# Optimization experiments

Measured on AMD Instinct MI355X. Metric: run time of the kernel, lower is better.

## Reference

```python
import jax, jax.numpy as jnp
import numpy as np

H, D = 8, 16            # num_heads, head_size
IN = H * D              # hgt_in_dim = 128
NT, ET = 3, 4           # node types, edge types (hard-coded in module)
N_DRUG, N_DIS, N_PROT = 10000, 10000, 30000
N = N_DRUG + N_DIS + N_PROT
E = 400000
LAYERS = 2
SQRT_D = float(np.sqrt(D))

# homogeneous node-type vector (presorted by type, as dgl.to_homogeneous yields)
NTYPE = jnp.concatenate([
    jnp.zeros(N_DRUG, jnp.int32),
    jnp.ones(N_DIS, jnp.int32),
    jnp.full((N_PROT,), 2, jnp.int32),
])


def typed_linear(x, types, W):
    # x: (M, in), W: (T, in, out), types: (M,) -> y[m] = x[m] @ W[types[m]]
    out = jnp.zeros((x.shape[0], W.shape[2]), x.dtype)
    for t in range(W.shape[0]):
        out = out + jnp.where((types == t)[:, None], x @ W[t], 0.0)
    return out


def hgt_conv(x, src, dst, etype, Wk, Wq, Wv, Wa, rel_att, rel_msg, pri, skip):
    # type-specific K/Q/V projections
    k = typed_linear(x, NTYPE, Wk).reshape(N, H, D)
    q = typed_linear(x, NTYPE, Wq).reshape(N, H, D)
    v = typed_linear(x, NTYPE, Wv).reshape(N, H, D)
    ke, qe, ve = k[src], q[dst], v[src]          # (E, H, D) gathers

    # per-edge-type relation transforms (vectorized over heads)
    kw = jnp.zeros_like(ke)
    mw = jnp.zeros_like(ve)
    for t in range(ET):
        sel = (etype == t)[:, None, None]
        kw = kw + jnp.where(sel, jnp.einsum('ehd,hdo->eho', ke, rel_att[:, t]), 0.0)
        mw = mw + jnp.where(sel, jnp.einsum('ehd,hdo->eho', ve, rel_msg[:, t]), 0.0)

    # attention logits: (kw . q) * relation_pri[head, etype] / sqrt(D)
    a = (kw * qe).sum(-1) * pri.T[etype] / SQRT_D  # (E, H)

    # edge softmax grouped by destination node, per head
    amax = jax.ops.segment_max(a, dst, num_segments=N)      # (N, H)
    ea = jnp.exp(a - amax[dst])
    esum = jax.ops.segment_sum(ea, dst, num_segments=N)
    attn = ea / esum[dst]                                   # (E, H)

    # weighted message aggregation (scatter-add over dst)
    m = mw * attn[..., None]                                 # (E, H, D)
    h = jax.ops.segment_sum(m, dst, num_segments=N).reshape(N, IN)

    # output projection (dropout = identity in eval) + sigmoid-skip residual
    h = typed_linear(h, NTYPE, Wa)
    alpha = jax.nn.sigmoid(skip)[NTYPE][:, None]
    return h * alpha + x * (1.0 - alpha)


def setup_inputs() -> dict:
    key = jax.random.key(0)
    ks = jax.random.split(key, 12)
    s = 0.05
    return {
        "drug_feature": jax.random.normal(ks[0], (N_DRUG, IN), jnp.float32),
        "disease_feature": jax.random.normal(ks[1], (N_DIS, IN), jnp.float32),
        "protein_feature": jax.random.normal(ks[2], (N_PROT, IN), jnp.float32),
        "src": jax.random.randint(ks[3], (E,), 0, N, dtype=jnp.int32),
        "dst": jax.random.randint(ks[4], (E,), 0, N, dtype=jnp.int32),
        "etype": jnp.sort(jax.random.randint(ks[5], (E,), 0, ET, dtype=jnp.int32)),
        "Wk": jax.random.normal(ks[6], (NT, IN, IN), jnp.float32) * s,
        "Wq": jax.random.normal(ks[7], (NT, IN, IN), jnp.float32) * s,
        "Wv": jax.random.normal(ks[8], (NT, IN, IN), jnp.float32) * s,
        "Wa": jax.random.normal(ks[9], (NT, IN, IN), jnp.float32) * s,
        "rel_att": jax.random.normal(ks[10], (H, ET, D, D), jnp.float32) * 0.1,
        "rel_msg": jax.random.normal(ks[11], (H, ET, D, D), jnp.float32) * 0.1,
        "pri": jnp.ones((H, ET), jnp.float32),
        "skip": jnp.ones((NT,), jnp.float32),
    }


def reference(drug_feature, disease_feature, protein_feature, src, dst, etype,
              Wk, Wq, Wv, Wa, rel_att, rel_msg, pri, skip):
    x = jnp.concatenate([drug_feature, disease_feature, protein_feature], axis=0)
    # ModuleList holds the SAME conv instance -> shared weights across layers
    for _ in range(LAYERS):
        x = hgt_conv(x, src, dst, etype, Wk, Wq, Wv, Wa, rel_att, rel_msg, pri, skip)
    return x
```

## Files before the change

### kernel.cpp

```cpp
#include <hip/hip_runtime.h>

#define N_NODE 50000
#define N_EDGE 400000
#define INF    128

#define FUSED_BLOCKS 1536

#define TILES0 313
#define TILES1 313
#define TILES2 938
#define PTILES 1564
#define PBLOCKS2 782

#define SB_CONCAT 2048
#define SB_COUNT  1563
#define SB_TWT    768
#define SB_TRMSG  32
#define SB_TOTAL  (SB_CONCAT + SB_COUNT + SB_TWT + SB_TRMSG)

typedef __bf16 bf16x8 __attribute__((ext_vector_type(8)));
typedef float  f32x4  __attribute__((ext_vector_type(4)));

__device__ __forceinline__ void seg_decode(int b, int& ty, int& base, int& nrows) {
  if (b < TILES0)            { ty = 0; base = b * 32;                      nrows = 10000 - base; }
  else if (b < TILES0+TILES1){ ty = 1; base = 10000 + (b - TILES0) * 32;   nrows = 20000 - base; }
  else                       { ty = 2; base = 20000 + (b - TILES0-TILES1)*32; nrows = 50000 - base; }
  if (nrows > 32) nrows = 32;
}

__device__ __forceinline__ float blo(unsigned u) { return __uint_as_float(u << 16); }
__device__ __forceinline__ float bhi(unsigned u) { return __uint_as_float(u & 0xffff0000u); }
__device__ __forceinline__ unsigned bpack(float lo, float hi) {
  unsigned a = __float_as_uint(lo), b = __float_as_uint(hi);
  a = (a + 0x7fffu + ((a >> 16) & 1u)) >> 16;
  b = (b + 0x7fffu + ((b >> 16) & 1u)) & 0xffff0000u;
  return a | b;
}
__device__ __forceinline__ unsigned short b16(float v) {
  unsigned u = __float_as_uint(v);
  return (unsigned short)((u + 0x7fffu + ((u >> 16) & 1u)) >> 16);
}
__device__ __forceinline__ bf16x8 ld_frag(const unsigned short* p) {
  uint4 u = *reinterpret_cast<const uint4*>(p);
  return __builtin_bit_cast(bf16x8, u);
}

__global__ __launch_bounds__(256) void k_setup(const float* __restrict__ dr,
                                               const float* __restrict__ di,
                                               const float* __restrict__ pr,
                                               float* __restrict__ x,
                                               unsigned short* __restrict__ xh,
                                               const int* __restrict__ dst,
                                               int* __restrict__ deg,
                                               const float* __restrict__ Wk,
                                               const float* __restrict__ Wq,
                                               const float* __restrict__ Wv,
                                               const float* __restrict__ Wa,
                                               unsigned short* __restrict__ WT,
                                               const float* __restrict__ rm,
                                               float* __restrict__ AmT) {
  int b = blockIdx.x;
  if (b < SB_CONCAT) {
    for (int i = b * 256 + threadIdx.x; i < N_NODE * 32; i += SB_CONCAT * 256) {
      int row = i >> 5;
      float4 val;
      if (row < 10000)      val = ((const float4*)dr)[i];
      else if (row < 20000) val = ((const float4*)di)[i - 10000*32];
      else                  val = ((const float4*)pr)[i - 20000*32];
      ((float4*)x)[i] = val;
      ((uint2*)xh)[i] = make_uint2(bpack(val.x, val.y), bpack(val.z, val.w));
    }
  } else if (b < SB_CONCAT + SB_COUNT) {
    int e = (b - SB_CONCAT) * 256 + threadIdx.x;
    if (e < N_EDGE) atomicAdd(&deg[dst[e]], 1);
  } else if (b < SB_CONCAT + SB_COUNT + SB_TWT) {
    int idx = (b - SB_CONCAT - SB_COUNT) * 256 + threadIdx.x;
    if (idx < 196608) {
      int mt = idx >> 14;
      int within = idx & 16383;
      int o = within >> 7, ii = within & 127;
      int mat = mt / 3, ty = mt % 3;
      const float* W = (mat == 0) ? Wk : (mat == 1) ? Wq : (mat == 2) ? Wv : Wa;
      WT[idx] = b16(W[ty * 16384 + ii * 128 + o]);
    }
  } else {
    int i = (b - SB_CONCAT - SB_COUNT - SB_TWT) * 256 + threadIdx.x;
    int di2 = i & 15, doo = (i >> 4) & 15, ty = (i >> 8) & 3, hh = i >> 10;
    AmT[i] = rm[((hh * 4 + ty) * 16 + di2) * 16 + doo];
  }
}

__global__ __launch_bounds__(1024) void k_scan(const int* __restrict__ deg,
                                               int* __restrict__ off, int* __restrict__ cur) {
  __shared__ int part[1024];
  int t = threadIdx.x;
  int c0 = t * 49;
  int c1 = c0 + 49; if (c1 > N_NODE) c1 = N_NODE;
  int s = 0;
  for (int i = c0; i < c1; ++i) s += deg[i];
  part[t] = s;
  __syncthreads();
  for (int ofs = 1; ofs < 1024; ofs <<= 1) {
    int v = (t >= ofs) ? part[t - ofs] : 0;
    __syncthreads();
    part[t] += v;
    __syncthreads();
  }
  int run = (t == 0) ? 0 : part[t - 1];
  for (int i = c0; i < c1; ++i) { off[i] = run; cur[i] = run; run += deg[i]; }
  if (t == 1023) off[N_NODE] = part[1023];
}

__global__ __launch_bounds__(256) void k_fill(const int* __restrict__ dst,
                                              const int* __restrict__ src,
                                              const int* __restrict__ etp,
                                              int* __restrict__ cur, int* __restrict__ est) {
  int e = blockIdx.x * 256 + threadIdx.x;
  if (e < N_EDGE) {
    int p = atomicAdd(&cur[dst[e]], 1);
    est[p] = (src[e] << 2) | etp[e];
  } else if (e < N_EDGE + 64) {
    est[e] = 0;
  }
}

__global__ __launch_bounds__(256) void k_qkv(const unsigned short* __restrict__ xh,
                                             const unsigned short* __restrict__ WT,
                                             const float* __restrict__ rel_att,
                                             const float* __restrict__ pri,
                                             uint2* __restrict__ kvb,
                                             uint4* __restrict__ qab) {
  __shared__ unsigned short qsh[2][32][136];
  int w = threadIdx.x >> 6, l = threadIdx.x & 63;
  int r16 = l & 15, ks = l >> 4;
  int t = w >> 1, ch = w & 1;
  int tile = blockIdx.x * 2 + t;
  int ty, base, wrows;
  seg_decode(tile, ty, base, wrows);
  int row0 = base;

  bf16x8 a[2][4];
#pragma unroll
  for (int st = 0; st < 2; ++st) {
    const unsigned short* xrow = xh + (size_t)(row0 + st * 16 + r16) * 128 + ks * 8;
#pragma unroll
    for (int kk = 0; kk < 4; ++kk) a[st][kk] = ld_frag(xrow + kk * 32);
  }

  const unsigned short* WK = WT + (size_t)(0 * 3 + ty) * 16384;
  const unsigned short* WQ = WT + (size_t)(1 * 3 + ty) * 16384;
  const unsigned short* WV = WT + (size_t)(2 * 3 + ty) * 16384;

#pragma unroll 1
  for (int ct = ch * 4; ct < ch * 4 + 4; ++ct) {
    int o = ct * 16 + r16;
    bf16x8 fbk[4], fbq[4], fbv[4];
#pragma unroll
    for (int kk = 0; kk < 4; ++kk) {
      fbk[kk] = ld_frag(WK + (size_t)o * 128 + ks * 8 + kk * 32);
      fbq[kk] = ld_frag(WQ + (size_t)o * 128 + ks * 8 + kk * 32);
      fbv[kk] = ld_frag(WV + (size_t)o * 128 + ks * 8 + kk * 32);
    }
#pragma unroll
    for (int st = 0; st < 2; ++st) {
      f32x4 ak = {0.f,0.f,0.f,0.f}, aq = {0.f,0.f,0.f,0.f}, av = {0.f,0.f,0.f,0.f};
#pragma unroll
      for (int kk = 0; kk < 4; ++kk) {
        ak = __builtin_amdgcn_mfma_f32_16x16x32_bf16(a[st][kk], fbk[kk], ak, 0, 0, 0);
        aq = __builtin_amdgcn_mfma_f32_16x16x32_bf16(a[st][kk], fbq[kk], aq, 0, 0, 0);
        av = __builtin_amdgcn_mfma_f32_16x16x32_bf16(a[st][kk], fbv[kk], av, 0, 0, 0);
      }
#pragma unroll
      for (int r = 0; r < 4; ++r) {
        int rrel = st * 16 + ks * 4 + r;
        float kn = __shfl_xor(ak[r], 1);
        float vn = __shfl_xor(av[r], 1);
        qsh[t][rrel][o] = b16(aq[r]);
        if (rrel < wrows && (l & 1) == 0) {
          size_t p = (size_t)(row0 + rrel);
          kvb[p * 64 + (o >> 1)] = make_uint2(bpack(ak[r], kn), bpack(av[r], vn));
        }
      }
    }
  }
  __syncthreads();

  int h = l >> 3, j = l & 7;
  float4 prh = ((const float4*)pri)[h];
  float prs[4] = { prh.x * 0.25f, prh.y * 0.25f, prh.z * 0.25f, prh.w * 0.25f };
  int nd0 = ch * 16;
  int lim = wrows - nd0; if (lim > 16) lim = 16;
  for (int i = 0; i < lim; ++i) {
    int nd = nd0 + i;
    unsigned u[8];
    *(uint4*)&u[0] = *(uint4*)&qsh[t][nd][h * 16 + 0];
    *(uint4*)&u[4] = *(uint4*)&qsh[t][nd][h * 16 + 8];
    float qf[16];
#pragma unroll
    for (int q2 = 0; q2 < 8; ++q2) { qf[2*q2] = blo(u[q2]); qf[2*q2+1] = bhi(u[q2]); }
    unsigned pk[4];
#pragma unroll
    for (int t4 = 0; t4 < 4; ++t4) {
      const float* Ar = rel_att + (((h * 4 + t4) * 16) + 2 * j) * 16;
      float ax = 0.f, ay = 0.f;
#pragma unroll
      for (int o = 0; o < 16; ++o) {
        ax += Ar[o] * qf[o];
        ay += Ar[16 + o] * qf[o];
      }
      pk[t4] = bpack(ax * prs[t4], ay * prs[t4]);
    }
    qab[(size_t)(row0 + nd) * 64 + l] = make_uint4(pk[0], pk[1], pk[2], pk[3]);
  }
}

__global__ __launch_bounds__(256)
__attribute__((amdgpu_waves_per_eu(3, 6)))
void k_fused(const uint2* __restrict__ kvb,
             const uint4* __restrict__ qab,
             const int* __restrict__ off,
             const int* __restrict__ est,
             const float* __restrict__ AmT,
             unsigned* __restrict__ hbh) {
  __shared__ float accs[4][4][128];
  int w = threadIdx.x >> 6, l = threadIdx.x & 63;
  int h = l >> 3, j = l & 7;

  for (int n = blockIdx.x * 4 + w; n < N_NODE; n += FUSED_BLOCKS * 4) {
    int o0 = off[n], o1 = off[n + 1];

    uint4 qu = qab[(size_t)n * 64 + l];
    float2 qa0 = make_float2(blo(qu.x), bhi(qu.x));
    float2 qa1 = make_float2(blo(qu.y), bhi(qu.y));
    float2 qa2 = make_float2(blo(qu.z), bhi(qu.z));
    float2 qa3 = make_float2(blo(qu.w), bhi(qu.w));

    float ssum = 0.f;
    float2 z = make_float2(0.f, 0.f);
    float2 at0 = z, at1 = z, at2 = z, at3 = z;

#define PROC(KV, TY, VALID) { \
    int ty = (TY) & 3; \
    float kx = blo((KV).x), ky = bhi((KV).x); \
    float2 qat = (ty==0)?qa0:(ty==1)?qa1:(ty==2)?qa2:qa3; \
    float part = kx*qat.x + ky*qat.y; \
    part += __shfl_xor(part, 1); \
    part += __shfl_xor(part, 2); \
    part += __shfl_xor(part, 4); \
    float wgt = (VALID) ? __expf(part) : 0.f; \
    ssum += wgt; \
    float vx = blo((KV).y), vy = bhi((KV).y); \
    float w0=(ty==0)?wgt:0.f, w1=(ty==1)?wgt:0.f, w2=(ty==2)?wgt:0.f, w3=(ty==3)?wgt:0.f; \
    at0.x += w0*vx; at0.y += w0*vy; \
    at1.x += w1*vx; at1.y += w1*vy; \
    at2.x += w2*vx; at2.y += w2*vy; \
    at3.x += w3*vx; at3.y += w3*vy; }

    for (int b0 = o0; b0 < o1; b0 += 64) {
      int cnt = o1 - b0; if (cnt > 64) cnt = 64;
      int stv = est[b0 + (l < cnt ? l : cnt - 1)];
      int t0 = __shfl(stv, 0);
      int t1 = __shfl(stv, 1 < cnt ? 1 : 0);
      uint2 kv0 = kvb[(size_t)(t0 >> 2) * 64 + l];
      uint2 kv1 = kvb[(size_t)(t1 >> 2) * 64 + l];
      for (int i = 0; i < cnt; i += 2) {
        bool more = (i + 2) < cnt;
        int n0 = 0, n1 = 0; uint2 kn0, kn1;
        if (more) {
          n0 = __shfl(stv, i + 2);
          n1 = __shfl(stv, (i + 3) < cnt ? (i + 3) : (i + 2));
          kn0 = kvb[(size_t)(n0 >> 2) * 64 + l];
          kn1 = kvb[(size_t)(n1 >> 2) * 64 + l];
        }
        PROC(kv0, t0, true)
        PROC(kv1, t1, (i + 1) < cnt)
        if (more) { t0 = n0; t1 = n1; kv0 = kn0; kv1 = kn1; }
      }
    }
#undef PROC

    float inv = (ssum > 0.f) ? 1.f / ssum : 0.f;
    at0.x *= inv; at0.y *= inv;
    at1.x *= inv; at1.y *= inv;
    at2.x *= inv; at2.y *= inv;
    at3.x *= inv; at3.y *= inv;

    ((float2*)&accs[w][0][0])[l] = at0;
    ((float2*)&accs[w][1][0])[l] = at1;
    ((float2*)&accs[w][2][0])[l] = at2;
    ((float2*)&accs[w][3][0])[l] = at3;

    float ox = 0.f, oy = 0.f;
#pragma unroll
    for (int ty = 0; ty < 4; ++ty) {
      const float4* AmR = (const float4*)(AmT + ((h * 4 + ty) * 16) * 16);
#pragma unroll
      for (int d4 = 0; d4 < 4; ++d4) {
        float4 ac = *((float4*)&accs[w][ty][h * 16 + d4 * 4]);
        float4 m0 = AmR[(2 * j) * 4 + d4];
        float4 m1 = AmR[(2 * j + 1) * 4 + d4];
        ox += m0.x * ac.x + m0.y * ac.y + m0.z * ac.z + m0.w * ac.w;
        oy += m1.x * ac.x + m1.y * ac.y + m1.z * ac.z + m1.w * ac.w;
      }
    }
    hbh[(size_t)n * 64 + l] = bpack(ox, oy);
  }
}

__global__ __launch_bounds__(256) void k_outqkv(const unsigned short* __restrict__ hbh,
                                                const unsigned short* __restrict__ WT,
                                                const float* __restrict__ skipv,
                                                const float* __restrict__ rel_att,
                                                const float* __restrict__ pri,
                                                float* __restrict__ xio,
                                                uint2* __restrict__ kvb,
                                                uint4* __restrict__ qab) {
  __shared__ unsigned short qsh[2][32][136];
  int w = threadIdx.x >> 6, l = threadIdx.x & 63;
  int r16 = l & 15, ks = l >> 4;
  int t = w >> 1, ch = w & 1;
  int tile = blockIdx.x * 2 + t;
  int ty, base, wrows;
  seg_decode(tile, ty, base, wrows);
  int row0 = base;

  {
    bf16x8 a[2][4];
#pragma unroll
    for (int st = 0; st < 2; ++st) {
      const unsigned short* hrow = hbh + (size_t)(row0 + st * 16 + r16) * 128 + ks * 8;
#pragma unroll
      for (int kk = 0; kk < 4; ++kk) a[st][kk] = ld_frag(hrow + kk * 32);
    }
    const unsigned short* WA = WT + (size_t)(3 * 3 + ty) * 16384;
    float alpha = 1.f / (1.f + __expf(-skipv[ty]));
    float beta = 1.f - alpha;
#pragma unroll 1
    for (int ct = ch * 4; ct < ch * 4 + 4; ++ct) {
      int o = ct * 16 + r16;
      bf16x8 ba[4];
#pragma unroll
      for (int kk = 0; kk < 4; ++kk)
        ba[kk] = ld_frag(WA + (size_t)o * 128 + ks * 8 + kk * 32);
#pragma unroll
      for (int st = 0; st < 2; ++st) {
        f32x4 acc = {0.f,0.f,0.f,0.f};
#pragma unroll
        for (int kk = 0; kk < 4; ++kk)
          acc = __builtin_amdgcn_mfma_f32_16x16x32_bf16(a[st][kk], ba[kk], acc, 0, 0, 0);
#pragma unroll
        for (int r = 0; r < 4; ++r) {
          int rrel = st * 16 + ks * 4 + r;
          size_t p = (size_t)(row0 + rrel) * 128 + o;
          float nx = 0.f;
          if (rrel < wrows) {
            nx = acc[r] * alpha + xio[p] * beta;
            xio[p] = nx;
          }
          qsh[t][rrel][o] = b16(nx);
        }
      }
    }
  }
  __syncthreads();

  bf16x8 a[2][4];
#pragma unroll
  for (int st = 0; st < 2; ++st)
#pragma unroll
    for (int kk = 0; kk < 4; ++kk)
      a[st][kk] = ld_frag(&qsh[t][st * 16 + r16][ks * 8 + kk * 32]);
  __syncthreads();

  const unsigned short* WK = WT + (size_t)(0 * 3 + ty) * 16384;
  const unsigned short* WQ = WT + (size_t)(1 * 3 + ty) * 16384;
  const unsigned short* WV = WT + (size_t)(2 * 3 + ty) * 16384;
#pragma unroll 1
  for (int ct = ch * 4; ct < ch * 4 + 4; ++ct) {
    int o = ct * 16 + r16;
    bf16x8 fbk[4], fbq[4], fbv[4];
#pragma unroll
    for (int kk = 0; kk < 4; ++kk) {
      fbk[kk] = ld_frag(WK + (size_t)o * 128 + ks * 8 + kk * 32);
      fbq[kk] = ld_frag(WQ + (size_t)o * 128 + ks * 8 + kk * 32);
      fbv[kk] = ld_frag(WV + (size_t)o * 128 + ks * 8 + kk * 32);
    }
#pragma unroll
    for (int st = 0; st < 2; ++st) {
      f32x4 ak = {0.f,0.f,0.f,0.f}, aq = {0.f,0.f,0.f,0.f}, av = {0.f,0.f,0.f,0.f};
#pragma unroll
      for (int kk = 0; kk < 4; ++kk) {
        ak = __builtin_amdgcn_mfma_f32_16x16x32_bf16(a[st][kk], fbk[kk], ak, 0, 0, 0);
        aq = __builtin_amdgcn_mfma_f32_16x16x32_bf16(a[st][kk], fbq[kk], aq, 0, 0, 0);
        av = __builtin_amdgcn_mfma_f32_16x16x32_bf16(a[st][kk], fbv[kk], av, 0, 0, 0);
      }
#pragma unroll
      for (int r = 0; r < 4; ++r) {
        int rrel = st * 16 + ks * 4 + r;
        float kn = __shfl_xor(ak[r], 1);
        float vn = __shfl_xor(av[r], 1);
        qsh[t][rrel][o] = b16(aq[r]);
        if (rrel < wrows && (l & 1) == 0) {
          size_t p = (size_t)(row0 + rrel);
          kvb[p * 64 + (o >> 1)] = make_uint2(bpack(ak[r], kn), bpack(av[r], vn));
        }
      }
    }
  }
  __syncthreads();

  int h = l >> 3, j = l & 7;
  float4 prh = ((const float4*)pri)[h];
  float prs[4] = { prh.x * 0.25f, prh.y * 0.25f, prh.z * 0.25f, prh.w * 0.25f };
  int nd0 = ch * 16;
  int lim = wrows - nd0; if (lim > 16) lim = 16;
  for (int i = 0; i < lim; ++i) {
    int nd = nd0 + i;
    unsigned u[8];
    *(uint4*)&u[0] = *(uint4*)&qsh[t][nd][h * 16 + 0];
    *(uint4*)&u[4] = *(uint4*)&qsh[t][nd][h * 16 + 8];
    float qf[16];
#pragma unroll
    for (int q2 = 0; q2 < 8; ++q2) { qf[2*q2] = blo(u[q2]); qf[2*q2+1] = bhi(u[q2]); }
    unsigned pk[4];
#pragma unroll
    for (int t4 = 0; t4 < 4; ++t4) {
      const float* Ar = rel_att + (((h * 4 + t4) * 16) + 2 * j) * 16;
      float ax = 0.f, ay = 0.f;
#pragma unroll
      for (int o = 0; o < 16; ++o) {
        ax += Ar[o] * qf[o];
        ay += Ar[16 + o] * qf[o];
      }
      pk[t4] = bpack(ax * prs[t4], ay * prs[t4]);
    }
    qab[(size_t)(row0 + nd) * 64 + l] = make_uint4(pk[0], pk[1], pk[2], pk[3]);
  }
}

__global__ __launch_bounds__(256) void k_out(const unsigned short* __restrict__ hbh,
                                             const unsigned short* __restrict__ WT,
                                             const float* __restrict__ skipv,
                                             float* __restrict__ xio) {
  int w = threadIdx.x >> 6, l = threadIdx.x & 63;
  int r16 = l & 15, ks = l >> 4;
  int t = w >> 1, ch = w & 1;
  int tile = blockIdx.x * 2 + t;
  int ty, base, wrows;
  seg_decode(tile, ty, base, wrows);
  int row0 = base;

  bf16x8 a[2][4];
#pragma unroll
  for (int st = 0; st < 2; ++st) {
    const unsigned short* hrow = hbh + (size_t)(row0 + st * 16 + r16) * 128 + ks * 8;
#pragma unroll
    for (int kk = 0; kk < 4; ++kk) a[st][kk] = ld_frag(hrow + kk * 32);
  }

  const unsigned short* WA = WT + (size_t)(3 * 3 + ty) * 16384;
  float alpha = 1.f / (1.f + __expf(-skipv[ty]));
  float beta = 1.f - alpha;

#pragma unroll 1
  for (int ct = ch * 4; ct < ch * 4 + 4; ++ct) {
    int o = ct * 16 + r16;
    bf16x8 ba[4];
#pragma unroll
    for (int kk = 0; kk < 4; ++kk)
      ba[kk] = ld_frag(WA + (size_t)o * 128 + ks * 8 + kk * 32);
#pragma unroll
    for (int st = 0; st < 2; ++st) {
      f32x4 acc = {0.f,0.f,0.f,0.f};
#pragma unroll
      for (int kk = 0; kk < 4; ++kk)
        acc = __builtin_amdgcn_mfma_f32_16x16x32_bf16(a[st][kk], ba[kk], acc, 0, 0, 0);
#pragma unroll
      for (int r = 0; r < 4; ++r) {
        int rrel = st * 16 + ks * 4 + r;
        if (rrel < wrows) {
          size_t p = (size_t)(row0 + rrel) * 128 + o;
          xio[p] = acc[r] * alpha + xio[p] * beta;
        }
      }
    }
  }
}

extern "C" void kernel_launch(void* const* d_in, const int* in_sizes, int n_in,
                              void* d_out, int out_size, void* d_ws, size_t ws_size,
                              hipStream_t stream) {
  const float* drug = (const float*)d_in[0];
  const float* dis  = (const float*)d_in[1];
  const float* prot = (const float*)d_in[2];
  const int* src    = (const int*)d_in[3];
  const int* dst    = (const int*)d_in[4];
  const int* etp    = (const int*)d_in[5];
  const float* Wk   = (const float*)d_in[6];
  const float* Wq   = (const float*)d_in[7];
  const float* Wv   = (const float*)d_in[8];
  const float* Wa   = (const float*)d_in[9];
  const float* rel_att = (const float*)d_in[10];
  const float* rel_msg = (const float*)d_in[11];
  const float* pri  = (const float*)d_in[12];
  const float* skip = (const float*)d_in[13];
  float* x = (float*)d_out;

  char* w = (char*)d_ws;
  uint2*          kvb = (uint2*)(w + 0);
  unsigned*       hbh = (unsigned*)(w + 25600000);
  uint4*          qab = (uint4*)(w + 38400000);
  unsigned short* xh  = (unsigned short*)(w + 89600000);
  unsigned short* WT  = (unsigned short*)(w + 102400000);
  float*          AmT = (float*)(w + 102793216);
  int*            off = (int*)(w + 102825984);
  int*            est = (int*)(w + 103026048);
  int*            deg = (int*)(w + 25600000);
  int*            cur = (int*)(w + 25800064);

  (void)hipMemsetAsync(deg, 0, N_NODE * sizeof(int), stream);
  k_setup<<<SB_TOTAL, 256, 0, stream>>>(drug, dis, prot, x, xh, dst, deg,
                                        Wk, Wq, Wv, Wa, WT, rel_msg, AmT);
  k_scan<<<1, 1024, 0, stream>>>(deg, off, cur);
  k_fill<<<(N_EDGE + 64 + 255) / 256, 256, 0, stream>>>(dst, src, etp, cur, est);

  k_qkv<<<PBLOCKS2, 256, 0, stream>>>(xh, WT, rel_att, pri, kvb, qab);
  k_fused<<<FUSED_BLOCKS, 256, 0, stream>>>(kvb, qab, off, est, AmT, hbh);
  k_outqkv<<<PBLOCKS2, 256, 0, stream>>>((const unsigned short*)hbh, WT, skip,
                                         rel_att, pri, x, kvb, qab);
  k_fused<<<FUSED_BLOCKS, 256, 0, stream>>>(kvb, qab, off, est, AmT, hbh);
  k_out<<<PBLOCKS2, 256, 0, stream>>>((const unsigned short*)hbh, WT, skip, x);
}
```

Measured before the change: 689.3 us.

## Process two destination nodes per wavefront with 32-lane halves and 16-byte gathers

The fused attention/aggregation kernel now splits each 64-lane wavefront into two 32-lane halves, each handling its own destination node. Every lane gathers a uint4 (four K and four V elements) per edge, so the dot-product reduction drops one shuffle stage, and the output projection computes four outputs per lane. The goal is to double per-lane work, widen memory transactions and cut per-node shuffle and loop overhead. The cost is divergence when the two nodes in a wave have different degrees, because the loop runs to the larger degree with masked edges. The est padding is also extended to 128 entries to cover the out-of-range reads that masked slots can make.

```diff
diff --git a/kernel.cpp b/kernel.cpp
--- a/kernel.cpp
+++ b/kernel.cpp
@@ -119,7 +119,7 @@
   if (e < N_EDGE) {
     int p = atomicAdd(&cur[dst[e]], 1);
     est[p] = (src[e] << 2) | etp[e];
-  } else if (e < N_EDGE + 64) {
+  } else if (e < N_EDGE + 128) {
     est[e] = 0;
   }
 }
@@ -222,88 +222,103 @@
              const int* __restrict__ est,
              const float* __restrict__ AmT,
              unsigned* __restrict__ hbh) {
-  __shared__ float accs[4][4][128];
+  __shared__ float accs[4][2][4][128];
+  const uint4* kv4 = (const uint4*)kvb;
   int w = threadIdx.x >> 6, l = threadIdx.x & 63;
-  int h = l >> 3, j = l & 7;
-
-  for (int n = blockIdx.x * 4 + w; n < N_NODE; n += FUSED_BLOCKS * 4) {
+  int half = l >> 5, m = l & 31;
+  int h = m >> 2, q4 = (m & 3) * 4;
+  int hbase = l & 32;
+
+  for (int nb = blockIdx.x * 8 + w * 2; nb < N_NODE; nb += FUSED_BLOCKS * 8) {
+    int n = nb + half;
     int o0 = off[n], o1 = off[n + 1];
-
-    uint4 qu = qab[(size_t)n * 64 + l];
-    float2 qa0 = make_float2(blo(qu.x), bhi(qu.x));
-    float2 qa1 = make_float2(blo(qu.y), bhi(qu.y));
-    float2 qa2 = make_float2(blo(qu.z), bhi(qu.z));
-    float2 qa3 = make_float2(blo(qu.w), bhi(qu.w));
+    int deg = o1 - o0;
+    int degmax = max(deg, __shfl_xor(deg, 32));
+
+    uint4 qu0 = qab[(size_t)n * 64 + 2 * m];
+    uint4 qu1 = qab[(size_t)n * 64 + 2 * m + 1];
+    float4 qa0 = make_float4(blo(qu0.x), bhi(qu0.x), blo(qu1.x), bhi(qu1.x));
+    float4 qa1 = make_float4(blo(qu0.y), bhi(qu0.y), blo(qu1.y), bhi(qu1.y));
+    float4 qa2 = make_float4(blo(qu0.z), bhi(qu0.z), blo(qu1.z), bhi(qu1.z));
+    float4 qa3 = make_float4(blo(qu0.w), bhi(qu0.w), blo(qu1.w), bhi(qu1.w));
 
     float ssum = 0.f;
-    float2 z = make_float2(0.f, 0.f);
-    float2 at0 = z, at1 = z, at2 = z, at3 = z;
-
-#define PROC(KV, TY, VALID) { \
-    int ty = (TY) & 3; \
-    float kx = blo((KV).x), ky = bhi((KV).x); \
-    float2 qat = (ty==0)?qa0:(ty==1)?qa1:(ty==2)?qa2:qa3; \
-    float part = kx*qat.x + ky*qat.y; \
+    float4 z = make_float4(0.f, 0.f, 0.f, 0.f);
+    float4 at0 = z, at1 = z, at2 = z, at3 = z;
+
+#define PROC(KV, T, VALID) { \
+    int ty = (T) & 3; \
+    float k0 = blo((KV).x), k1 = bhi((KV).x), k2 = blo((KV).z), k3 = bhi((KV).z); \
+    float4 qat = (ty==0)?qa0:(ty==1)?qa1:(ty==2)?qa2:qa3; \
+    float part = k0*qat.x + k1*qat.y + k2*qat.z + k3*qat.w; \
     part += __shfl_xor(part, 1); \
     part += __shfl_xor(part, 2); \
-    part += __shfl_xor(part, 4); \
     float wgt = (VALID) ? __expf(part) : 0.f; \
     ssum += wgt; \
-    float vx = blo((KV).y), vy = bhi((KV).y); \
+    float v0 = blo((KV).y), v1 = bhi((KV).y), v2 = blo((KV).w), v3 = bhi((KV).w); \
     float w0=(ty==0)?wgt:0.f, w1=(ty==1)?wgt:0.f, w2=(ty==2)?wgt:0.f, w3=(ty==3)?wgt:0.f; \
-    at0.x += w0*vx; at0.y += w0*vy; \
-    at1.x += w1*vx; at1.y += w1*vy; \
-    at2.x += w2*vx; at2.y += w2*vy; \
-    at3.x += w3*vx; at3.y += w3*vy; }
-
-    for (int b0 = o0; b0 < o1; b0 += 64) {
-      int cnt = o1 - b0; if (cnt > 64) cnt = 64;
-      int stv = est[b0 + (l < cnt ? l : cnt - 1)];
-      int t0 = __shfl(stv, 0);
-      int t1 = __shfl(stv, 1 < cnt ? 1 : 0);
-      uint2 kv0 = kvb[(size_t)(t0 >> 2) * 64 + l];
-      uint2 kv1 = kvb[(size_t)(t1 >> 2) * 64 + l];
-      for (int i = 0; i < cnt; i += 2) {
-        bool more = (i + 2) < cnt;
-        int n0 = 0, n1 = 0; uint2 kn0, kn1;
+    at0.x += w0*v0; at0.y += w0*v1; at0.z += w0*v2; at0.w += w0*v3; \
+    at1.x += w1*v0; at1.y += w1*v1; at1.z += w1*v2; at1.w += w1*v3; \
+    at2.x += w2*v0; at2.y += w2*v1; at2.z += w2*v2; at2.w += w2*v3; \
+    at3.x += w3*v0; at3.y += w3*v1; at3.z += w3*v2; at3.w += w3*v3; }
+
+    for (int b0 = 0; b0 < degmax; b0 += 32) {
+      int cnt = deg - b0; if (cnt > 32) cnt = 32; if (cnt < 0) cnt = 0;
+      int cmax = degmax - b0; if (cmax > 32) cmax = 32;
+      int cidx = (cnt > 0) ? (m < cnt ? m : cnt - 1) : 0;
+      int stv = est[o0 + b0 + cidx];
+#define SLOT(I) (((I) < cnt) ? (I) : (cnt > 0 ? cnt - 1 : 0))
+      int t0 = __shfl(stv, hbase + SLOT(0));
+      int t1 = __shfl(stv, hbase + SLOT(1));
+      uint4 kv0 = kv4[(size_t)(t0 >> 2) * 32 + m];
+      uint4 kv1 = kv4[(size_t)(t1 >> 2) * 32 + m];
+      for (int i = 0; i < cmax; i += 2) {
+        bool more = (i + 2) < cmax;
+        int n0 = 0, n1 = 0; uint4 kn0, kn1;
         if (more) {
-          n0 = __shfl(stv, i + 2);
-          n1 = __shfl(stv, (i + 3) < cnt ? (i + 3) : (i + 2));
-          kn0 = kvb[(size_t)(n0 >> 2) * 64 + l];
-          kn1 = kvb[(size_t)(n1 >> 2) * 64 + l];
+          n0 = __shfl(stv, hbase + SLOT(i + 2));
+          n1 = __shfl(stv, hbase + SLOT(i + 3));
+          kn0 = kv4[(size_t)(n0 >> 2) * 32 + m];
+          kn1 = kv4[(size_t)(n1 >> 2) * 32 + m];
         }
-        PROC(kv0, t0, true)
+        PROC(kv0, t0, i < cnt)
         PROC(kv1, t1, (i + 1) < cnt)
         if (more) { t0 = n0; t1 = n1; kv0 = kn0; kv1 = kn1; }
       }
+#undef SLOT
     }
 #undef PROC
 
     float inv = (ssum > 0.f) ? 1.f / ssum : 0.f;
-    at0.x *= inv; at0.y *= inv;
-    at1.x *= inv; at1.y *= inv;
-    at2.x *= inv; at2.y *= inv;
-    at3.x *= inv; at3.y *= inv;
-
-    ((float2*)&accs[w][0][0])[l] = at0;
-    ((float2*)&accs[w][1][0])[l] = at1;
-    ((float2*)&accs[w][2][0])[l] = at2;
-    ((float2*)&accs[w][3][0])[l] = at3;
-
-    float ox = 0.f, oy = 0.f;
+    at0.x *= inv; at0.y *= inv; at0.z *= inv; at0.w *= inv;
+    at1.x *= inv; at1.y *= inv; at1.z *= inv; at1.w *= inv;
+    at2.x *= inv; at2.y *= inv; at2.z *= inv; at2.w *= inv;
+    at3.x *= inv; at3.y *= inv; at3.z *= inv; at3.w *= inv;
+
+    ((float4*)&accs[w][half][0][0])[m] = at0;
+    ((float4*)&accs[w][half][1][0])[m] = at1;
+    ((float4*)&accs[w][half][2][0])[m] = at2;
+    ((float4*)&accs[w][half][3][0])[m] = at3;
+
+    float o0v = 0.f, o1v = 0.f, o2v = 0.f, o3v = 0.f;
 #pragma unroll
     for (int ty = 0; ty < 4; ++ty) {
-      const float4* AmR = (const float4*)(AmT + ((h * 4 + ty) * 16) * 16);
-#pragma unroll
-      for (int d4 = 0; d4 < 4; ++d4) {
-        float4 ac = *((float4*)&accs[w][ty][h * 16 + d4 * 4]);
-        float4 m0 = AmR[(2 * j) * 4 + d4];
-        float4 m1 = AmR[(2 * j + 1) * 4 + d4];
-        ox += m0.x * ac.x + m0.y * ac.y + m0.z * ac.z + m0.w * ac.w;
-        oy += m1.x * ac.x + m1.y * ac.y + m1.z * ac.z + m1.w * ac.w;
-      }
-    }
-    hbh[(size_t)n * 64 + l] = bpack(ox, oy);
+      float4 c0 = *(float4*)&accs[w][half][ty][16 * h + 0];
+      float4 c1 = *(float4*)&accs[w][half][ty][16 * h + 4];
+      float4 c2 = *(float4*)&accs[w][half][ty][16 * h + 8];
+      float4 c3 = *(float4*)&accs[w][half][ty][16 * h + 12];
+      const float4* AmR = (const float4*)(AmT + ((size_t)((h * 4 + ty) * 16 + q4)) * 16);
+#define ROWDOT(R) (AmR[(R)*4+0].x*c0.x + AmR[(R)*4+0].y*c0.y + AmR[(R)*4+0].z*c0.z + AmR[(R)*4+0].w*c0.w \
+                 + AmR[(R)*4+1].x*c1.x + AmR[(R)*4+1].y*c1.y + AmR[(R)*4+1].z*c1.z + AmR[(R)*4+1].w*c1.w \
+                 + AmR[(R)*4+2].x*c2.x + AmR[(R)*4+2].y*c2.y + AmR[(R)*4+2].z*c2.z + AmR[(R)*4+2].w*c2.w \
+                 + AmR[(R)*4+3].x*c3.x + AmR[(R)*4+3].y*c3.y + AmR[(R)*4+3].z*c3.z + AmR[(R)*4+3].w*c3.w)
+      o0v += ROWDOT(0);
+      o1v += ROWDOT(1);
+      o2v += ROWDOT(2);
+      o3v += ROWDOT(3);
+#undef ROWDOT
+    }
+    ((uint2*)hbh)[(size_t)n * 32 + m] = make_uint2(bpack(o0v, o1v), bpack(o2v, o3v));
   }
 }
 
@@ -522,7 +537,7 @@
   k_setup<<<SB_TOTAL, 256, 0, stream>>>(drug, dis, prot, x, xh, dst, deg,
                                         Wk, Wq, Wv, Wa, WT, rel_msg, AmT);
   k_scan<<<1, 1024, 0, stream>>>(deg, off, cur);
-  k_fill<<<(N_EDGE + 64 + 255) / 256, 256, 0, stream>>>(dst, src, etp, cur, est);
+  k_fill<<<(N_EDGE + 128 + 255) / 256, 256, 0, stream>>>(dst, src, etp, cur, est);
 
   k_qkv<<<PBLOCKS2, 256, 0, stream>>>(xh, WT, rel_att, pri, kvb, qab);
   k_fused<<<FUSED_BLOCKS, 256, 0, stream>>>(kvb, qab, off, est, AmT, hbh);
```

Result: slower. 1.311 ms (+90.2%).
